# Performance work log

Measured on AMD Instinct MI355X. Metric: run time of the kernel, lower is better.

The kernel has to match this reference:

```python
import jax, jax.numpy as jnp
import numpy as np

B, T, D, E, C = 4, 4096, 2048, 8, 1024
H = D // E  # per-expert hidden = out_features // num_experts = 256


def setup_inputs() -> dict:
    key = jax.random.key(0)
    ks = jax.random.split(key, 7)
    x = jax.random.normal(ks[0], (B, T, D), dtype=jnp.float32)
    # nn.Linear-style init scale ~ 1/sqrt(fan_in)
    W1 = jax.random.normal(ks[1], (E, H, D), dtype=jnp.float32) / np.sqrt(D)
    b1 = jax.random.normal(ks[2], (E, H), dtype=jnp.float32) / np.sqrt(D)
    W2 = jax.random.normal(ks[3], (E, D, H), dtype=jnp.float32) / np.sqrt(D)
    b2 = jax.random.normal(ks[4], (D,), dtype=jnp.float32) / np.sqrt(D)
    expert_indices = jax.random.randint(ks[5], (B, E, C), 0, T, dtype=jnp.int32)
    expert_gate = jax.random.uniform(ks[6], (B, E, C), dtype=jnp.float32)
    return {"x": x, "W1": W1, "b1": b1, "W2": W2, "b2": b2,
            "expert_indices": expert_indices, "expert_gate": expert_gate,
            "num_tokens": T}


def reference(x, W1, b1, W2, b2, expert_indices, expert_gate, num_tokens):
    # x: (B,T,D); expert_indices/expert_gate: (B,E,C)
    Bb = x.shape[0]
    Ee, Cc = expert_indices.shape[1], expert_indices.shape[2]
    b_idx = jnp.arange(Bb)[:, None, None]
    # dispatch: gather tokens per expert -> (B,E,C,D)
    sel = x[b_idx, expert_indices]
    # contract: per-expert GEMM -> (B,E,C,H)
    h = jnp.einsum('becd,ehd->bech', sel, W1) + b1[None, :, None, :]
    h = jax.nn.gelu(h, approximate=False)
    # expand: per-expert GEMM -> (B,E,C,D), shared output bias
    y = jnp.einsum('bech,eoh->beco', h, W2) + b2
    y = y * expert_gate[..., None]
    # combine: gated scatter-add back to token positions -> (B,T,D)
    out = jnp.zeros((Bb, num_tokens, x.shape[2]), dtype=x.dtype)
    out = out.at[jnp.arange(Bb)[:, None], expert_indices.reshape(Bb, Ee * Cc)].add(
        y.reshape(Bb, Ee * Cc, -1))
    return out
```

## Files before the change

kernel.cpp:

```cpp
#include <hip/hip_runtime.h>
#include <hip/hip_bf16.h>
#include <math.h>

#define B_ 4
#define T_ 4096
#define D_ 2048
#define E_ 8
#define C_ 1024
#define H_ 256
#define SLOTCAP 32

typedef unsigned short u16;
typedef unsigned long long u64;
typedef __attribute__((ext_vector_type(8))) short short8;
typedef __attribute__((ext_vector_type(4))) float f32x4;

__device__ __forceinline__ u16 f2bf_n(float f) {
    union { __hip_bfloat16 b; u16 u; } v;
    v.b = __float2bfloat16(f);
    return v.u;
}
__device__ __forceinline__ float bf2f(u16 u) {
    union { unsigned u; float f; } v; v.u = ((unsigned)u) << 16;
    return v.f;
}

__device__ __forceinline__ int swz(int row, int chunk) {
    return (row << 6) + ((chunk ^ (row & 7)) << 3);
}

__device__ __forceinline__ void gload16(const void* g, void* l) {
    __builtin_amdgcn_global_load_lds(
        (const __attribute__((address_space(1))) void*)g,
        (__attribute__((address_space(3))) void*)l, 16, 0, 0);
}

__global__ __launch_bounds__(256) void conv_x_bf16(
    const float* __restrict__ src, u16* __restrict__ dst, int n)
{
    int i = (blockIdx.x * 256 + threadIdx.x) * 4;
    if (i >= n) return;
    f32x4 v = *reinterpret_cast<const f32x4*>(src + i);
    u16 o[4];
    o[0] = f2bf_n(v[0]); o[1] = f2bf_n(v[1]); o[2] = f2bf_n(v[2]); o[3] = f2bf_n(v[3]);
    *reinterpret_cast<u64*>(dst + i) = *reinterpret_cast<const u64*>(o);
}

__global__ __launch_bounds__(256) void conv_w1_img(
    const float* __restrict__ W1, u16* __restrict__ img)
{
    const int cid = blockIdx.x * 256 + threadIdx.x;
    const int e = cid >> 16;
    const int kt = (cid >> 11) & 31;
    const int row = (cid >> 3) & 255;
    const int sc = cid & 7;
    const float* s = W1 + (((size_t)e * 256 + row) * 2048 + kt * 64
                           + ((sc ^ (row & 7)) << 3));
    f32x4 v0 = *reinterpret_cast<const f32x4*>(s);
    f32x4 v1 = *reinterpret_cast<const f32x4*>(s + 4);
    u16 o[8];
    #pragma unroll
    for (int j = 0; j < 4; ++j) { o[j] = f2bf_n(v0[j]); o[j + 4] = f2bf_n(v1[j]); }
    *reinterpret_cast<short8*>(img + (size_t)cid * 8) =
        *reinterpret_cast<const short8*>(o);
}

__global__ __launch_bounds__(256) void conv_w2_img(
    const float* __restrict__ W2, u16* __restrict__ img)
{
    const int cid = blockIdx.x * 256 + threadIdx.x;
    const int e = cid >> 16;
    const int nt = (cid >> 13) & 7;
    const int kt = (cid >> 11) & 3;
    const int row = (cid >> 3) & 255;
    const int sc = cid & 7;
    const float* s = W2 + (((size_t)e * 2048 + nt * 256 + row) * 256 + kt * 64
                           + ((sc ^ (row & 7)) << 3));
    f32x4 v0 = *reinterpret_cast<const f32x4*>(s);
    f32x4 v1 = *reinterpret_cast<const f32x4*>(s + 4);
    u16 o[8];
    #pragma unroll
    for (int j = 0; j < 4; ++j) { o[j] = f2bf_n(v0[j]); o[j + 4] = f2bf_n(v1[j]); }
    *reinterpret_cast<short8*>(img + (size_t)cid * 8) =
        *reinterpret_cast<const short8*>(o);
}

__global__ __launch_bounds__(512) void gemm1_v8(
    const u16* __restrict__ xbf, const u16* __restrict__ W1img,
    const float* __restrict__ b1, const int* __restrict__ idx,
    u16* __restrict__ Himg)
{
    const int be = blockIdx.x;
    const int mt = blockIdx.y;
    const int b = be >> 3, e = be & 7;
    const int m0 = mt * 64;

    __shared__ __align__(16) u16 As[2][4096];
    __shared__ __align__(16) u16 Bs[2][16384];

    const int tid = threadIdx.x;
    const int lane = tid & 63, wid = tid >> 6;
    const int wm = wid >> 2, wn = wid & 3;
    const int l15 = lane & 15, lk = lane >> 4;

    const int row8 = tid >> 3, asc = tid & 7;
    const int tok = idx[(b * E_ + e) * C_ + m0 + row8];
    const u16* aSrc = xbf + ((size_t)b * T_ + tok) * D_
                          + ((asc ^ (row8 & 7)) << 3);
    const u16* bSrc = W1img + (size_t)e * 32 * 16384 + (size_t)tid * 8;
    const int wofs = wid * 512;

#define G1_ISSUE(buf, t)                                                      \
    do {                                                                      \
        gload16(aSrc + (t) * 64, &As[buf][wofs]);                             \
        const u16* b_ = bSrc + (size_t)(t) * 16384;                           \
        gload16(b_,         &Bs[buf][wofs]);                                  \
        gload16(b_ + 4096,  &Bs[buf][4096 + wofs]);                           \
        gload16(b_ + 8192,  &Bs[buf][8192 + wofs]);                           \
        gload16(b_ + 12288, &Bs[buf][12288 + wofs]);                          \
    } while (0)

    f32x4 acc[2][4];
    #pragma unroll
    for (int i = 0; i < 2; ++i)
        #pragma unroll
        for (int j = 0; j < 4; ++j)
            acc[i][j] = (f32x4){0.f, 0.f, 0.f, 0.f};

    G1_ISSUE(0, 0);
    G1_ISSUE(1, 1);

    const int NT = D_ / 64;
    for (int t = 0; t < NT; ++t) {
        const int cur = t & 1;
        if (t < NT - 1) asm volatile("s_waitcnt vmcnt(5)" ::: "memory");
        else            asm volatile("s_waitcnt vmcnt(0)" ::: "memory");
        __builtin_amdgcn_s_barrier();
        __builtin_amdgcn_sched_barrier(0);
        #pragma unroll
        for (int kk = 0; kk < 2; ++kk) {
            short8 af[2], bfr[4];
            #pragma unroll
            for (int m = 0; m < 2; ++m) {
                const int row = wm * 32 + m * 16 + l15;
                af[m] = *reinterpret_cast<const short8*>(
                    &As[cur][swz(row, kk * 4 + lk)]);
            }
            #pragma unroll
            for (int n = 0; n < 4; ++n) {
                const int row = wn * 64 + n * 16 + l15;
                bfr[n] = *reinterpret_cast<const short8*>(
                    &Bs[cur][swz(row, kk * 4 + lk)]);
            }
            __builtin_amdgcn_s_setprio(1);
            #pragma unroll
            for (int m = 0; m < 2; ++m)
                #pragma unroll
                for (int n = 0; n < 4; ++n)
                    acc[m][n] = __builtin_amdgcn_mfma_f32_16x16x32_bf16(
                        bfr[n], af[m], acc[m][n], 0, 0, 0);
            __builtin_amdgcn_s_setprio(0);
        }
        asm volatile("s_waitcnt lgkmcnt(0)" ::: "memory");
        __builtin_amdgcn_s_barrier();
        __builtin_amdgcn_sched_barrier(0);
        if (t + 2 < NT) G1_ISSUE(cur, t + 2);
    }
#undef G1_ISSUE

    const size_t hblk = ((size_t)(be * 16 + mt) * 4 + wn) * 4096;
    #pragma unroll
    for (int m = 0; m < 2; ++m) {
        const int row = wm * 32 + m * 16 + l15;
        #pragma unroll
        for (int n = 0; n < 4; ++n) {
            const int hb = wn * 64 + n * 16 + lk * 4;
            f32x4 bias = *reinterpret_cast<const f32x4*>(&b1[e * H_ + hb]);
            u16 o[4];
            #pragma unroll
            for (int r = 0; r < 4; ++r) {
                float h = acc[m][n][r] + bias[r];
                float g = 0.5f * h * (1.0f + erff(h * 0.70710678118f));
                o[r] = f2bf_n(g);
            }
            const int lc = (n * 2 + (lk >> 1)) ^ (row & 7);
            u16* p = Himg + hblk + row * 64 + lc * 8 + (lk & 1) * 4;
            *reinterpret_cast<u64*>(p) = *reinterpret_cast<const u64*>(o);
        }
    }
}

__global__ __launch_bounds__(512) void gemm2_v7(
    const u16* __restrict__ Himg, const u16* __restrict__ W2img,
    const float* __restrict__ b2, const float* __restrict__ gate,
    u16* __restrict__ Ybuf)
{
    const int be = blockIdx.x;
    const int nt = blockIdx.y;
    const int b = be >> 3, e = be & 7;
    const int n0 = nt * 256;

    __shared__ __align__(16) u16 As[16384];
    __shared__ __align__(16) u16 Bs[65536];

    const int tid = threadIdx.x;
    const int lane = tid & 63, wid = tid >> 6;
    const int wm = wid >> 2, wn = wid & 3;
    const int l15 = lane & 15, lk = lane >> 4;
    const int wofs = wid * 512;

    const u16* bPanel = W2img + (size_t)(e * 8 + nt) * 65536;
    #pragma unroll
    for (int j = 0; j < 16; ++j)
        gload16(bPanel + (size_t)(j * 512 + tid) * 8, &Bs[j * 4096 + wofs]);

    const u16* aBase = Himg + (size_t)(be * 16) * 16384 + (size_t)tid * 8;

#define A_ISSUE(mt)                                                           \
    do {                                                                      \
        const u16* a_ = aBase + (size_t)(mt) * 16384;                         \
        gload16(a_,          &As[wofs]);                                      \
        gload16(a_ + 4096,   &As[4096 + wofs]);                               \
        gload16(a_ + 8192,   &As[8192 + wofs]);                               \
        gload16(a_ + 12288,  &As[12288 + wofs]);                              \
    } while (0)

    A_ISSUE(0);

    f32x4 bias[4];
    #pragma unroll
    for (int n = 0; n < 4; ++n)
        bias[n] = *reinterpret_cast<const f32x4*>(
            &b2[n0 + wn * 64 + n * 16 + lk * 4]);

    const int gbase = (b * E_ + e) * C_;
    const size_t ybase = (size_t)(b * E_ + e) * C_;

    asm volatile("s_waitcnt vmcnt(0)" ::: "memory");
    __builtin_amdgcn_s_barrier();
    __builtin_amdgcn_sched_barrier(0);

    for (int mt = 0; mt < 16; ++mt) {
        f32x4 acc[2][4];
        #pragma unroll
        for (int i = 0; i < 2; ++i)
            #pragma unroll
            for (int j = 0; j < 4; ++j)
                acc[i][j] = (f32x4){0.f, 0.f, 0.f, 0.f};

        #pragma unroll
        for (int t = 0; t < 4; ++t) {
            #pragma unroll
            for (int kk = 0; kk < 2; ++kk) {
                short8 af[2], bfr[4];
                #pragma unroll
                for (int m = 0; m < 2; ++m) {
                    const int row = wm * 32 + m * 16 + l15;
                    af[m] = *reinterpret_cast<const short8*>(
                        &As[t * 4096 + swz(row, kk * 4 + lk)]);
                }
                #pragma unroll
                for (int n = 0; n < 4; ++n) {
                    const int row = wn * 64 + n * 16 + l15;
                    bfr[n] = *reinterpret_cast<const short8*>(
                        &Bs[t * 16384 + swz(row, kk * 4 + lk)]);
                }
                __builtin_amdgcn_s_setprio(1);
                #pragma unroll
                for (int m = 0; m < 2; ++m)
                    #pragma unroll
                    for (int n = 0; n < 4; ++n)
                        acc[m][n] = __builtin_amdgcn_mfma_f32_16x16x32_bf16(
                            bfr[n], af[m], acc[m][n], 0, 0, 0);
                __builtin_amdgcn_s_setprio(0);
            }
        }

        asm volatile("s_waitcnt lgkmcnt(0)" ::: "memory");
        __builtin_amdgcn_s_barrier();
        __builtin_amdgcn_sched_barrier(0);

        const float g0 = gate[gbase + mt * 64 + wm * 32 + l15];
        const float g1 = gate[gbase + mt * 64 + wm * 32 + 16 + l15];
        if (mt < 15) A_ISSUE(mt + 1);

        #pragma unroll
        for (int m = 0; m < 2; ++m) {
            const int cl = wm * 32 + m * 16 + l15;
            const float g = (m == 0) ? g0 : g1;
            u16* rowp = Ybuf + (ybase + mt * 64 + cl) * (size_t)D_ + n0;
            #pragma unroll
            for (int n = 0; n < 4; ++n) {
                const int db = wn * 64 + n * 16 + lk * 4;
                u16 o[4];
                #pragma unroll
                for (int r = 0; r < 4; ++r)
                    o[r] = f2bf_n((acc[m][n][r] + bias[n][r]) * g);
                *reinterpret_cast<u64*>(rowp + db) =
                    *reinterpret_cast<const u64*>(o);
            }
        }

        if (mt < 15) {
            asm volatile("s_waitcnt vmcnt(8)" ::: "memory");
            __builtin_amdgcn_s_barrier();
            __builtin_amdgcn_sched_barrier(0);
        }
    }
#undef A_ISSUE
}

__global__ __launch_bounds__(256) void fill_kernel(
    const int* __restrict__ idx, int* __restrict__ cnt,
    int* __restrict__ slots)
{
    int i = blockIdx.x * 256 + threadIdx.x;
    if (i >= B_ * E_ * C_) return;
    int b = i / (E_ * C_);
    int slot = i % (E_ * C_);
    int t = idx[i];
    int p = atomicAdd(&cnt[b * T_ + t], 1);
    if (p < SLOTCAP) slots[(b * T_ + t) * SLOTCAP + p] = slot;
}

__global__ __launch_bounds__(256) void combine_kernel(
    const u16* __restrict__ Ybuf, const int* __restrict__ cnt,
    const int* __restrict__ slots, float* __restrict__ out)
{
    const int bt = blockIdx.x;
    const int tid = threadIdx.x;
    __shared__ int sl[SLOTCAP];
    int n = cnt[bt];
    n = n > SLOTCAP ? SLOTCAP : n;
    if (tid < n) sl[tid] = slots[bt * SLOTCAP + tid];
    __syncthreads();
    const int b = bt >> 12;
    float a[8] = {0.f, 0.f, 0.f, 0.f, 0.f, 0.f, 0.f, 0.f};
    for (int s = 0; s < n; ++s) {
        const u16* yrow = Ybuf + ((size_t)b * (E_ * C_) + sl[s]) * D_ + tid * 8;
        short8 v = *reinterpret_cast<const short8*>(yrow);
        #pragma unroll
        for (int j = 0; j < 8; ++j) a[j] += bf2f((u16)v[j]);
    }
    float* orow = out + (size_t)bt * D_ + tid * 8;
    *reinterpret_cast<f32x4*>(orow)     = (f32x4){a[0], a[1], a[2], a[3]};
    *reinterpret_cast<f32x4*>(orow + 4) = (f32x4){a[4], a[5], a[6], a[7]};
}

extern "C" void kernel_launch(void* const* d_in, const int* in_sizes, int n_in,
                              void* d_out, int out_size, void* d_ws, size_t ws_size,
                              hipStream_t stream) {
    const float* x    = (const float*)d_in[0];
    const float* W1   = (const float*)d_in[1];
    const float* b1   = (const float*)d_in[2];
    const float* W2   = (const float*)d_in[3];
    const float* b2   = (const float*)d_in[4];
    const int*   idx  = (const int*)d_in[5];
    const float* gate = (const float*)d_in[6];
    float* out = (float*)d_out;

    const size_t nW = (size_t)E_ * H_ * D_;
    const size_t nX = (size_t)B_ * T_ * D_;
    const size_t nH = (size_t)B_ * E_ * C_ * H_;
    const size_t nY = (size_t)B_ * E_ * C_ * D_;

    u16* W1img = (u16*)d_ws;
    u16* W2img = W1img + nW;
    u16* Himg  = W2img + nW;
    u16* Ybuf  = Himg + nH;
    u16* xbf   = Ybuf;
    int* cnt   = (int*)(Ybuf + nY);
    int* slots = cnt + (size_t)B_ * T_;

    hipMemsetAsync(cnt, 0, (size_t)B_ * T_ * sizeof(int), stream);
    conv_w1_img<<<2048, 256, 0, stream>>>(W1, W1img);
    conv_w2_img<<<2048, 256, 0, stream>>>(W2, W2img);
    conv_x_bf16<<<(int)(nX / 1024), 256, 0, stream>>>(x, xbf, (int)nX);
    fill_kernel<<<(B_ * E_ * C_) / 256, 256, 0, stream>>>(idx, cnt, slots);

    gemm1_v8<<<dim3(32, 16), 512, 0, stream>>>(xbf, W1img, b1, idx, Himg);
    gemm2_v7<<<dim3(32, 8), 512, 0, stream>>>(Himg, W2img, b2, gate, Ybuf);
    combine_kernel<<<B_ * T_, 256, 0, stream>>>(Ybuf, cnt, slots, out);
}
```

Baseline: 218.3 us.

## Fuse x fp32-to-bf16 conversion into gemm1 A-tile staging, drop conv_x kernel

Removes the standalone pass that converted all of x to bf16 and instead has gemm1 load the gathered fp32 token rows, convert them in registers, and write them swizzled into LDS. This avoids reading and writing the full x tensor once, which is significant since only gathered rows are needed. In exchange, the A-tile path becomes a synchronous register round trip with twice the global bytes per gathered row, and waitcnt accounting changes. The memset of the counter buffer is also replaced with a small zeroing kernel.

New measurement: 215.5 us. About the same (-1.3%).

```diff
diff --git a/kernel.cpp b/kernel.cpp
--- a/kernel.cpp
+++ b/kernel.cpp
@@ -33,17 +33,6 @@
     __builtin_amdgcn_global_load_lds(
         (const __attribute__((address_space(1))) void*)g,
         (__attribute__((address_space(3))) void*)l, 16, 0, 0);
-}
-
-__global__ __launch_bounds__(256) void conv_x_bf16(
-    const float* __restrict__ src, u16* __restrict__ dst, int n)
-{
-    int i = (blockIdx.x * 256 + threadIdx.x) * 4;
-    if (i >= n) return;
-    f32x4 v = *reinterpret_cast<const f32x4*>(src + i);
-    u16 o[4];
-    o[0] = f2bf_n(v[0]); o[1] = f2bf_n(v[1]); o[2] = f2bf_n(v[2]); o[3] = f2bf_n(v[3]);
-    *reinterpret_cast<u64*>(dst + i) = *reinterpret_cast<const u64*>(o);
 }
 
 __global__ __launch_bounds__(256) void conv_w1_img(
@@ -85,8 +74,14 @@
         *reinterpret_cast<const short8*>(o);
 }
 
-__global__ __launch_bounds__(512) void gemm1_v8(
-    const u16* __restrict__ xbf, const u16* __restrict__ W1img,
+__global__ __launch_bounds__(256) void zero_cnt(int* __restrict__ cnt)
+{
+    const int i = (blockIdx.x * 256 + threadIdx.x) * 4;
+    *reinterpret_cast<f32x4*>(cnt + i) = (f32x4){0.f, 0.f, 0.f, 0.f};
+}
+
+__global__ __launch_bounds__(512) void gemm1_v9(
+    const float* __restrict__ x, const u16* __restrict__ W1img,
     const float* __restrict__ b1, const int* __restrict__ idx,
     u16* __restrict__ Himg)
 {
@@ -105,14 +100,14 @@
 
     const int row8 = tid >> 3, asc = tid & 7;
     const int tok = idx[(b * E_ + e) * C_ + m0 + row8];
-    const u16* aSrc = xbf + ((size_t)b * T_ + tok) * D_
-                          + ((asc ^ (row8 & 7)) << 3);
+    const float* aRow = x + ((size_t)b * T_ + tok) * D_ + asc * 8;
+    const int aOff = swz(row8, asc);
+
     const u16* bSrc = W1img + (size_t)e * 32 * 16384 + (size_t)tid * 8;
     const int wofs = wid * 512;
 
-#define G1_ISSUE(buf, t)                                                      \
+#define B_ISSUE(buf, t)                                                       \
     do {                                                                      \
-        gload16(aSrc + (t) * 64, &As[buf][wofs]);                             \
         const u16* b_ = bSrc + (size_t)(t) * 16384;                           \
         gload16(b_,         &Bs[buf][wofs]);                                  \
         gload16(b_ + 4096,  &Bs[buf][4096 + wofs]);                           \
@@ -120,6 +115,18 @@
         gload16(b_ + 12288, &Bs[buf][12288 + wofs]);                          \
     } while (0)
 
+#define A_STAGE(buf, t)                                                       \
+    do {                                                                      \
+        f32x4 v0 = *reinterpret_cast<const f32x4*>(aRow + (t) * 64);          \
+        f32x4 v1 = *reinterpret_cast<const f32x4*>(aRow + (t) * 64 + 4);      \
+        short8 s;                                                             \
+        _Pragma("unroll")                                                     \
+        for (int r = 0; r < 4; ++r) {                                         \
+            s[r] = (short)f2bf_n(v0[r]); s[r + 4] = (short)f2bf_n(v1[r]);     \
+        }                                                                     \
+        *reinterpret_cast<short8*>(&As[buf][aOff]) = s;                       \
+    } while (0)
+
     f32x4 acc[2][4];
     #pragma unroll
     for (int i = 0; i < 2; ++i)
@@ -127,13 +134,16 @@
         for (int j = 0; j < 4; ++j)
             acc[i][j] = (f32x4){0.f, 0.f, 0.f, 0.f};
 
-    G1_ISSUE(0, 0);
-    G1_ISSUE(1, 1);
+    B_ISSUE(0, 0);
+    B_ISSUE(1, 1);
+    A_STAGE(0, 0);
+    A_STAGE(1, 1);
+    asm volatile("s_waitcnt lgkmcnt(0)" ::: "memory");
 
     const int NT = D_ / 64;
     for (int t = 0; t < NT; ++t) {
         const int cur = t & 1;
-        if (t < NT - 1) asm volatile("s_waitcnt vmcnt(5)" ::: "memory");
+        if (t < NT - 1) asm volatile("s_waitcnt vmcnt(4)" ::: "memory");
         else            asm volatile("s_waitcnt vmcnt(0)" ::: "memory");
         __builtin_amdgcn_s_barrier();
         __builtin_amdgcn_sched_barrier(0);
@@ -164,9 +174,13 @@
         asm volatile("s_waitcnt lgkmcnt(0)" ::: "memory");
         __builtin_amdgcn_s_barrier();
         __builtin_amdgcn_sched_barrier(0);
-        if (t + 2 < NT) G1_ISSUE(cur, t + 2);
+        if (t + 2 < NT) {
+            B_ISSUE(cur, t + 2);
+            A_STAGE(cur, t + 2);
+        }
     }
-#undef G1_ISSUE
+#undef B_ISSUE
+#undef A_STAGE
 
     const size_t hblk = ((size_t)(be * 16 + mt) * 4 + wn) * 4096;
     #pragma unroll
@@ -360,7 +374,6 @@
     float* out = (float*)d_out;
 
     const size_t nW = (size_t)E_ * H_ * D_;
-    const size_t nX = (size_t)B_ * T_ * D_;
     const size_t nH = (size_t)B_ * E_ * C_ * H_;
     const size_t nY = (size_t)B_ * E_ * C_ * D_;
 
@@ -368,17 +381,15 @@
     u16* W2img = W1img + nW;
     u16* Himg  = W2img + nW;
     u16* Ybuf  = Himg + nH;
-    u16* xbf   = Ybuf;
     int* cnt   = (int*)(Ybuf + nY);
     int* slots = cnt + (size_t)B_ * T_;
 
-    hipMemsetAsync(cnt, 0, (size_t)B_ * T_ * sizeof(int), stream);
+    zero_cnt<<<(B_ * T_) / 1024, 256, 0, stream>>>(cnt);
     conv_w1_img<<<2048, 256, 0, stream>>>(W1, W1img);
     conv_w2_img<<<2048, 256, 0, stream>>>(W2, W2img);
-    conv_x_bf16<<<(int)(nX / 1024), 256, 0, stream>>>(x, xbf, (int)nX);
     fill_kernel<<<(B_ * E_ * C_) / 256, 256, 0, stream>>>(idx, cnt, slots);
 
-    gemm1_v8<<<dim3(32, 16), 512, 0, stream>>>(xbf, W1img, b1, idx, Himg);
+    gemm1_v9<<<dim3(32, 16), 512, 0, stream>>>(x, W1img, b1, idx, Himg);
     gemm2_v7<<<dim3(32, 8), 512, 0, stream>>>(Himg, W2img, b2, gate, Ybuf);
     combine_kernel<<<B_ * T_, 256, 0, stream>>>(Ybuf, cnt, slots, out);
 }
```
